# Kernel tuning notes

Measured on AMD Instinct MI355X. Metric: run time of the kernel, lower is better.

The kernel has to match this reference:

```python
import jax, jax.numpy as jnp
import numpy as np

ATT_HEAD, IN_DIM, OUT_DIM = 8, 768, 96
B, N = 8, 1024
LEAKY_ALPHA = 0.2


def setup_inputs() -> dict:
    key = jax.random.key(0)
    ks = jax.random.split(key, 8)
    feat_in = jax.random.normal(ks[0], (B, N, IN_DIM), dtype=jnp.float32)
    adj = jax.random.randint(ks[1], (B, N, N), 0, 2).astype(jnp.float32)
    # xavier-ish init scales
    W = jax.random.normal(ks[2], (ATT_HEAD, IN_DIM, OUT_DIM), dtype=jnp.float32) * (1.0 / np.sqrt(IN_DIM))
    b = jnp.zeros((OUT_DIM,), dtype=jnp.float32)
    w_src = jax.random.normal(ks[3], (ATT_HEAD, OUT_DIM, 1), dtype=jnp.float32) * (1.0 / np.sqrt(OUT_DIM))
    w_dst = jax.random.normal(ks[4], (ATT_HEAD, OUT_DIM, 1), dtype=jnp.float32) * (1.0 / np.sqrt(OUT_DIM))
    Hw = jax.random.normal(ks[5], (IN_DIM, IN_DIM), dtype=jnp.float32) * (1.0 / np.sqrt(IN_DIM))
    Hb = jnp.zeros((IN_DIM,), dtype=jnp.float32)
    return {"feat_in": feat_in, "adj": adj, "W": W, "b": b,
            "w_src": w_src, "w_dst": w_dst, "Hw": Hw, "Hb": Hb}


def reference(feat_in, adj, W, b, w_src, w_dst, Hw, Hb):
    batch, n, _ = feat_in.shape
    # per-head projection: [B,H,N,O]
    h = jnp.einsum('bni,hio->bhno', feat_in, W)
    t = jnp.tanh(h)
    a_src = jnp.einsum('bhno,hoq->bhnq', t, w_src)[..., 0]  # [B,H,N]
    a_dst = jnp.einsum('bhno,hoq->bhnq', t, w_dst)[..., 0]  # [B,H,N]
    attn = a_src[:, :, :, None] + a_dst[:, :, None, :]       # [B,H,N,N]
    attn = jnp.where(attn >= 0, attn, LEAKY_ALPHA * attn)
    mask = adj[:, None, :, :] == 0                            # 1-adj as bool
    attn = jnp.where(mask, jnp.float32(-999.0), attn)
    attn = jax.nn.softmax(attn, axis=-1)
    feat_out = jnp.einsum('bhnm,bhmo->bhno', attn, h) + b     # [B,H,N,O]
    feat_out = jnp.transpose(feat_out, (0, 2, 1, 3)).reshape(batch, n, -1)
    feat_out = jax.nn.elu(feat_out)
    gate = jax.nn.sigmoid(feat_in @ Hw.T + Hb)
    return gate * feat_out + (1.0 - gate) * feat_in
```

## Files before the change

kernel.cpp:

```cpp
#include <hip/hip_runtime.h>
#include <cstddef>

#define BATCH 8
#define NN 1024
#define IN_DIM 768
#define OUT_DIM 96
#define HEADS 8
#define M_ROWS 8192
#define NCOLS 1536

typedef __attribute__((ext_vector_type(8))) short short8;
typedef __attribute__((ext_vector_type(4))) float f32x4;
typedef __attribute__((ext_vector_type(4))) unsigned short ushort4v;
typedef _Float16 half8 __attribute__((ext_vector_type(8)));

typedef __attribute__((address_space(1))) void gvoid_t;
typedef __attribute__((address_space(3))) void lvoid_t;

__device__ __forceinline__ void gload_lds16(const void* g, void* l) {
    __builtin_amdgcn_global_load_lds((gvoid_t*)(unsigned long long)g,
                                     (lvoid_t*)(unsigned int)(unsigned long long)l,
                                     16, 0, 0);
}

__device__ __forceinline__ unsigned int pkrtz(float a, float b) {
    return __builtin_bit_cast(unsigned int, __builtin_amdgcn_cvt_pkrtz(a, b));
}
__device__ __forceinline__ unsigned short f2h(float x) {
    _Float16 h = (_Float16)x;
    return __builtin_bit_cast(unsigned short, h);
}
__device__ __forceinline__ float h2f(unsigned short u) {
    return (float)__builtin_bit_cast(_Float16, u);
}
__device__ __forceinline__ float tanh_fast(float x) {
    return 1.f - 2.f / (__expf(2.f * x) + 1.f);
}
__device__ __forceinline__ f32x4 mfma16(short8 a, short8 b, f32x4 c) {
    return __builtin_amdgcn_mfma_f32_16x16x32_f16(
        __builtin_bit_cast(half8, a), __builtin_bit_cast(half8, b), c, 0, 0, 0);
}

__global__ __launch_bounds__(256) void prep_kernel(
        const float* __restrict__ feat_in, const float* __restrict__ W,
        const float* __restrict__ Hw, const float* __restrict__ adj,
        unsigned short* __restrict__ Xb, unsigned short* __restrict__ BT,
        unsigned int* __restrict__ abits, float* __restrict__ a_zero) {
    int blk = blockIdx.x;
    int t = threadIdx.x;
    if (blk < 3072) {
        int idx = blk * 256 + t;
        const float4* p = (const float4*)(feat_in + (size_t)idx * 8);
        float4 a = p[0], b = p[1];
        union { unsigned int u4[4]; short8 s8; } pk;
        pk.u4[0] = pkrtz(a.x, a.y);
        pk.u4[1] = pkrtz(a.z, a.w);
        pk.u4[2] = pkrtz(b.x, b.y);
        pk.u4[3] = pkrtz(b.z, b.w);
        *(short8*)(Xb + (size_t)idx * 8) = pk.s8;
    } else if (blk < 5376) {
        int idx = (blk - 3072) * 256 + t;
        int c = idx / IN_DIM, i = idx % IN_DIM;
        int h = c / OUT_DIM, o = c % OUT_DIM;
        BT[(size_t)c * IN_DIM + i] = f2h(W[((size_t)h * IN_DIM + i) * OUT_DIM + o]);
    } else if (blk < 7680) {
        int idx = (blk - 5376) * 256 + t;
        int c = idx / IN_DIM, i = idx % IN_DIM;
        BT[(size_t)(768 + c) * IN_DIM + i] = f2h(Hw[(size_t)c * IN_DIM + i]);
    } else if (blk < 8704) {
        int idx = (blk - 7680) * 256 + t;
        const float4* p = (const float4*)(adj + (size_t)idx * 32);
        unsigned int m = 0;
        #pragma unroll
        for (int q = 0; q < 8; ++q) {
            float4 v = p[q];
            m |= (v.x != 0.f ? 1u : 0u) << (q * 4 + 0);
            m |= (v.y != 0.f ? 1u : 0u) << (q * 4 + 1);
            m |= (v.z != 0.f ? 1u : 0u) << (q * 4 + 2);
            m |= (v.w != 0.f ? 1u : 0u) << (q * 4 + 3);
        }
        abits[idx] = m;
    } else {
        int idx = (blk - 8704) * 256 + t;
        f32x4 z = {0.f, 0.f, 0.f, 0.f};
        *(f32x4*)(a_zero + (size_t)idx * 8) = z;
        *(f32x4*)(a_zero + (size_t)idx * 8 + 4) = z;
    }
}

__global__ __launch_bounds__(256) void gemm1_kernel(
        const unsigned short* __restrict__ Xb, const unsigned short* __restrict__ BT,
        const float* __restrict__ Hb, const float* __restrict__ w_src,
        const float* __restrict__ w_dst,
        unsigned short* __restrict__ h_bt, unsigned short* __restrict__ gate,
        float* __restrict__ a_src, float* __restrict__ a_dst) {
    __shared__ __align__(16) unsigned short As[128 * 64];
    __shared__ __align__(16) unsigned short Bs[128 * 64];
    __shared__ float hbs[128];
    __shared__ float ws_s[128], wd_s[128];
    int m0 = blockIdx.x * 128;
    int c0 = blockIdx.y * 128;
    int t = threadIdx.x;
    int w = t >> 6, lane = t & 63, l15 = t & 15, quad = lane >> 4;
    if (c0 >= 768) {
        if (t < 128) hbs[t] = Hb[c0 - 768 + t];
    } else {
        if (t < 128) {
            int c = c0 + t;
            int hd = c / OUT_DIM, o = c % OUT_DIM;
            ws_s[t] = w_src[hd * OUT_DIM + o];
            wd_s[t] = w_dst[hd * OUT_DIM + o];
        }
    }
    f32x4 acc[2][8] = {};
    for (int k0 = 0; k0 < IN_DIM; k0 += 64) {
        __syncthreads();
        #pragma unroll
        for (int cc = 0; cc < 4; ++cc) {
            int base64 = (w * 4 + cc) * 64;
            int p = base64 + lane;
            int r = p >> 3, qs = p & 7;
            int qb = qs ^ (r & 7);
            gload_lds16(Xb + (size_t)(m0 + r) * IN_DIM + k0 + qb * 8, As + base64 * 8);
            gload_lds16(BT + (size_t)(c0 + r) * IN_DIM + k0 + qb * 8, Bs + base64 * 8);
        }
        __syncthreads();
        #pragma unroll
        for (int ks = 0; ks < 2; ++ks) {
            short8 af[2], bfr[8];
            #pragma unroll
            for (int mt = 0; mt < 2; ++mt) {
                int r = w * 32 + mt * 16 + l15;
                int cb = (ks * 4 + quad) ^ (r & 7);
                af[mt] = *(const short8*)(As + r * 64 + cb * 8);
            }
            #pragma unroll
            for (int nt = 0; nt < 8; ++nt) {
                int r = nt * 16 + l15;
                int cb = (ks * 4 + quad) ^ (r & 7);
                bfr[nt] = *(const short8*)(Bs + r * 64 + cb * 8);
            }
            #pragma unroll
            for (int mt = 0; mt < 2; ++mt)
                #pragma unroll
                for (int nt = 0; nt < 8; ++nt)
                    acc[mt][nt] = mfma16(af[mt], bfr[nt], acc[mt][nt]);
        }
    }
    int b = m0 >> 10;
    if (c0 < 768) {
        int split = (c0 / 96 + 1) * 96 - c0;
        int headlo = c0 / 96;
        #pragma unroll
        for (int mt = 0; mt < 2; ++mt) {
            int rowbase = m0 + w * 32 + mt * 16 + quad * 4;
            int nbase = rowbase & 1023;
            #pragma unroll
            for (int nt = 0; nt < 8; ++nt) {
                int c = c0 + nt * 16 + l15;
                int hh = c / OUT_DIM, o = c % OUT_DIM;
                union { unsigned int u2[2]; ushort4v u4; } pk;
                pk.u2[0] = pkrtz(acc[mt][nt][0], acc[mt][nt][1]);
                pk.u2[1] = pkrtz(acc[mt][nt][2], acc[mt][nt][3]);
                *(ushort4v*)(h_bt + ((size_t)(b * 8 + hh) * OUT_DIM + o) * NN + nbase) = pk.u4;
            }
            #pragma unroll
            for (int reg = 0; reg < 4; ++reg) {
                float psA = 0.f, pdA = 0.f, psB = 0.f, pdB = 0.f;
                #pragma unroll
                for (int nt = 0; nt < 8; ++nt) {
                    int cl = nt * 16 + l15;
                    float th = tanh_fast(acc[mt][nt][reg]);
                    float s = th * ws_s[cl], d = th * wd_s[cl];
                    if (cl < split) { psA += s; pdA += d; }
                    else            { psB += s; pdB += d; }
                }
                #pragma unroll
                for (int mk = 1; mk <= 8; mk <<= 1) {
                    psA += __shfl_xor(psA, mk); pdA += __shfl_xor(pdA, mk);
                    psB += __shfl_xor(psB, mk); pdB += __shfl_xor(pdB, mk);
                }
                if (l15 == 0) {
                    int n2 = nbase + reg;
                    int ilo = (b * 8 + headlo) * 1024 + n2;
                    atomicAdd(&a_src[ilo], psA * 1.44269504f);
                    atomicAdd(&a_dst[ilo], pdA * 1.44269504f);
                    atomicAdd(&a_src[ilo + 1024], psB * 1.44269504f);
                    atomicAdd(&a_dst[ilo + 1024], pdB * 1.44269504f);
                }
            }
        }
    } else {
        #pragma unroll
        for (int mt = 0; mt < 2; ++mt) {
            int rowbase = m0 + w * 32 + mt * 16 + quad * 4;
            #pragma unroll
            for (int nt = 0; nt < 8; ++nt) {
                int cl = nt * 16 + l15;
                int cg = c0 - 768 + cl;
                #pragma unroll
                for (int reg = 0; reg < 4; ++reg) {
                    float z = acc[mt][nt][reg] + hbs[cl];
                    float g = __builtin_amdgcn_rcpf(1.f + __builtin_amdgcn_exp2f(-1.44269504f * z));
                    gate[(size_t)(rowbase + reg) * 768 + cg] = f2h(g);
                }
            }
        }
    }
}

__global__ __launch_bounds__(512) void attn_kernel(
        const unsigned short* __restrict__ h_bt, const unsigned int* __restrict__ abits,
        const float* __restrict__ a_src_g, const float* __restrict__ a_dst_g,
        const unsigned short* __restrict__ gate, const unsigned short* __restrict__ Xb,
        const float* __restrict__ bias, float* __restrict__ out) {
    __shared__ __align__(16) unsigned short hs[2][96 * 64];
    __shared__ __align__(16) float adst[1024];
    __shared__ float bias_s[96];
    int blk = blockIdx.x;
    int bh = (blk & 7) * 8 + ((blk >> 3) & 7);
    int i0 = (blk >> 6) * 128;
    int b = bh >> 3, hh = bh & 7;
    int t = threadIdx.x;
    int w = t >> 6, lane = t & 63, l15 = t & 15, quad = lane >> 4;
    if (t < 256) *(f32x4*)(adst + t * 4) = *(const f32x4*)(a_dst_g + bh * 1024 + t * 4);
    if (t < 96) bias_s[t] = bias[t];
    int irow = i0 + w * 16 + l15;
    float si = a_src_g[bh * 1024 + irow];
    const unsigned short* hhp = h_bt + (size_t)bh * 96 * NN;
    if (w < 6) {
        #pragma unroll
        for (int cc = 0; cc < 2; ++cc) {
            int u0 = (w * 2 + cc) * 64;
            int p = u0 + lane;
            int r = p >> 3, qs = p & 7, qb = qs ^ (r & 7);
            gload_lds16(hhp + (size_t)r * NN + qb * 8, (char*)&hs[0][0] + (size_t)u0 * 16);
        }
    }
    const unsigned int* mrow = abits + ((size_t)b * NN + irow) * 32;
    uint2 mw = *(const uint2*)(mrow);
    f32x4 acc[7] = {};
    short8 ones = {};
    if (l15 == 0) {
        #pragma unroll
        for (int u = 0; u < 8; ++u) ones[u] = (short)0x3C00;
    }
    __syncthreads();
    for (int j0 = 0; j0 < 1024; j0 += 64) {
        int cur = (j0 >> 6) & 1;
        int jn = j0 + 64;
        if (jn < 1024 && w < 6) {
            #pragma unroll
            for (int cc = 0; cc < 2; ++cc) {
                int u0 = (w * 2 + cc) * 64;
                int p = u0 + lane;
                int r = p >> 3, qs = p & 7, qb = qs ^ (r & 7);
                gload_lds16(hhp + (size_t)r * NN + jn + qb * 8, (char*)&hs[cur ^ 1][0] + (size_t)u0 * 16);
            }
        }
        short8 af[2];
        unsigned int mws[2] = {mw.x, mw.y};
        #pragma unroll
        for (int ks = 0; ks < 2; ++ks) {
            unsigned int byte = (mws[ks] >> (quad * 8)) & 0xFFu;
            f32x4 d0 = *(const f32x4*)(&adst[j0 + ks * 32 + quad * 8]);
            f32x4 d1 = *(const f32x4*)(&adst[j0 + ks * 32 + quad * 8 + 4]);
            float dv[8] = {d0[0], d0[1], d0[2], d0[3], d1[0], d1[1], d1[2], d1[3]};
            float ev[8];
            #pragma unroll
            for (int u = 0; u < 8; ++u) {
                float s = si + dv[u];
                float l = fmaxf(s, 0.2f * s);
                float e = __builtin_amdgcn_exp2f(l);
                ev[u] = ((byte >> u) & 1u) ? e : 0.f;
            }
            union { unsigned int u4[4]; short8 s8; } pk;
            pk.u4[0] = pkrtz(ev[0], ev[1]);
            pk.u4[1] = pkrtz(ev[2], ev[3]);
            pk.u4[2] = pkrtz(ev[4], ev[5]);
            pk.u4[3] = pkrtz(ev[6], ev[7]);
            af[ks] = pk.s8;
        }
        if (jn < 1024) mw = *(const uint2*)(mrow + (jn >> 5));
        #pragma unroll
        for (int ks = 0; ks < 2; ++ks) {
            #pragma unroll
            for (int nt = 0; nt < 6; ++nt) {
                int r = nt * 16 + l15;
                int qs = (ks * 4 + quad) ^ (r & 7);
                short8 bfr = *(const short8*)(&hs[cur][(size_t)(r * 8 + qs) * 8]);
                acc[nt] = mfma16(af[ks], bfr, acc[nt]);
            }
            acc[6] = mfma16(af[ks], ones, acc[6]);
        }
        __syncthreads();
    }
    int rowq = i0 + w * 16 + quad * 4;
    #pragma unroll
    for (int reg = 0; reg < 4; ++reg) {
        float ssum = __shfl(acc[6][reg], (lane & 48));
        float inv = (ssum > 0.f) ? __builtin_amdgcn_rcpf(ssum) : 0.f;
        int n = rowq + reg;
        size_t mrow_o = ((size_t)b * NN + n) * 768 + hh * 96;
        #pragma unroll
        for (int nt = 0; nt < 6; ++nt) {
            int cl = nt * 16 + l15;
            float v = acc[nt][reg] * inv + bias_s[cl];
            float e = (v > 0.f) ? v : (__builtin_amdgcn_exp2f(v * 1.44269504f) - 1.f);
            float g = h2f(gate[mrow_o + cl]);
            float x = h2f(Xb[mrow_o + cl]);
            out[mrow_o + cl] = x + g * (e - x);
        }
    }
}

extern "C" void kernel_launch(void* const* d_in, const int* in_sizes, int n_in,
                              void* d_out, int out_size, void* d_ws, size_t ws_size,
                              hipStream_t stream) {
    const float* feat_in = (const float*)d_in[0];
    const float* adj     = (const float*)d_in[1];
    const float* W       = (const float*)d_in[2];
    const float* bbias   = (const float*)d_in[3];
    const float* w_src   = (const float*)d_in[4];
    const float* w_dst   = (const float*)d_in[5];
    const float* Hw      = (const float*)d_in[6];
    const float* Hb      = (const float*)d_in[7];
    float* out = (float*)d_out;
    char* base = (char*)d_ws;

    unsigned short* Xb    = (unsigned short*)(base);
    unsigned short* BcatT = (unsigned short*)(base + 12582912);
    unsigned short* h_bt  = (unsigned short*)(base + 14942208);
    unsigned short* gate  = (unsigned short*)(base + 27525120);
    float* a_src = (float*)(base + 40108032);
    float* a_dst = (float*)(base + 40370176);
    unsigned int* abits = (unsigned int*)(base + 40632320);

    prep_kernel<<<8768, 256, 0, stream>>>(feat_in, W, Hw, adj, Xb, BcatT, abits, a_src);
    gemm1_kernel<<<dim3(M_ROWS / 128, NCOLS / 128), 256, 0, stream>>>(
        Xb, BcatT, Hb, w_src, w_dst, h_bt, gate, a_src, a_dst);
    attn_kernel<<<64 * 8, 512, 0, stream>>>(h_bt, abits, a_src, a_dst, gate, Xb, bbias, out);
}
```

Measured before the change: 185.3 us.

## Double-buffer gemm1 LDS tiles with 32-wide K steps to overlap loads

Replaces the single-buffered 64-wide K loop in gemm1 with two 32-wide LDS buffers. The global-to-LDS load for the next K slice is issued before the MFMA work on the current slice, so memory latency is meant to hide behind compute. The XOR swizzle is dropped in favour of an unswizzled 32-column layout, which may bring LDS bank conflicts back. The step count doubles and the number of barriers per unit of work goes up.

```diff
diff --git a/kernel.cpp b/kernel.cpp
--- a/kernel.cpp
+++ b/kernel.cpp
@@ -94,8 +94,8 @@
         const float* __restrict__ w_dst,
         unsigned short* __restrict__ h_bt, unsigned short* __restrict__ gate,
         float* __restrict__ a_src, float* __restrict__ a_dst) {
-    __shared__ __align__(16) unsigned short As[128 * 64];
-    __shared__ __align__(16) unsigned short Bs[128 * 64];
+    __shared__ __align__(16) unsigned short As[2][128 * 32];
+    __shared__ __align__(16) unsigned short Bs[2][128 * 32];
     __shared__ float hbs[128];
     __shared__ float ws_s[128], wd_s[128];
     int m0 = blockIdx.x * 128;
@@ -112,41 +112,47 @@
             wd_s[t] = w_dst[hd * OUT_DIM + o];
         }
     }
+    int uA0 = w * 2, uA1 = w * 2 + 1;
+    int rA0 = uA0 * 16 + (lane >> 2), rA1 = uA1 * 16 + (lane >> 2);
+    int qo = (lane & 3) * 8;
+    const unsigned short* gA0 = Xb + (size_t)(m0 + rA0) * IN_DIM + qo;
+    const unsigned short* gA1 = Xb + (size_t)(m0 + rA1) * IN_DIM + qo;
+    const unsigned short* gB0 = BT + (size_t)(c0 + rA0) * IN_DIM + qo;
+    const unsigned short* gB1 = BT + (size_t)(c0 + rA1) * IN_DIM + qo;
+    int aoff0 = (w * 32 + l15) * 32 + quad * 8;
+    int aoff1 = aoff0 + 16 * 32;
+    int boff  = l15 * 32 + quad * 8;
+
     f32x4 acc[2][8] = {};
-    for (int k0 = 0; k0 < IN_DIM; k0 += 64) {
+
+    auto stage = [&](unsigned short* Ad, unsigned short* Bd, int koff) {
+        gload_lds16(gA0 + koff, Ad + uA0 * 512);
+        gload_lds16(gA1 + koff, Ad + uA1 * 512);
+        gload_lds16(gB0 + koff, Bd + uA0 * 512);
+        gload_lds16(gB1 + koff, Bd + uA1 * 512);
+    };
+    auto compute = [&](const unsigned short* Ab, const unsigned short* Bb) {
+        short8 af0 = *(const short8*)(Ab + aoff0);
+        short8 af1 = *(const short8*)(Ab + aoff1);
+        #pragma unroll
+        for (int nt = 0; nt < 8; ++nt) {
+            short8 bfr = *(const short8*)(Bb + boff + nt * 512);
+            acc[0][nt] = mfma16(af0, bfr, acc[0][nt]);
+            acc[1][nt] = mfma16(af1, bfr, acc[1][nt]);
+        }
+    };
+
+    stage(&As[0][0], &Bs[0][0], 0);
+    __syncthreads();
+    for (int ts = 0; ts < 24; ts += 2) {
+        stage(&As[1][0], &Bs[1][0], (ts + 1) * 32);
+        compute(&As[0][0], &Bs[0][0]);
         __syncthreads();
-        #pragma unroll
-        for (int cc = 0; cc < 4; ++cc) {
-            int base64 = (w * 4 + cc) * 64;
-            int p = base64 + lane;
-            int r = p >> 3, qs = p & 7;
-            int qb = qs ^ (r & 7);
-            gload_lds16(Xb + (size_t)(m0 + r) * IN_DIM + k0 + qb * 8, As + base64 * 8);
-            gload_lds16(BT + (size_t)(c0 + r) * IN_DIM + k0 + qb * 8, Bs + base64 * 8);
-        }
+        if (ts + 2 < 24) stage(&As[0][0], &Bs[0][0], (ts + 2) * 32);
+        compute(&As[1][0], &Bs[1][0]);
         __syncthreads();
-        #pragma unroll
-        for (int ks = 0; ks < 2; ++ks) {
-            short8 af[2], bfr[8];
-            #pragma unroll
-            for (int mt = 0; mt < 2; ++mt) {
-                int r = w * 32 + mt * 16 + l15;
-                int cb = (ks * 4 + quad) ^ (r & 7);
-                af[mt] = *(const short8*)(As + r * 64 + cb * 8);
-            }
-            #pragma unroll
-            for (int nt = 0; nt < 8; ++nt) {
-                int r = nt * 16 + l15;
-                int cb = (ks * 4 + quad) ^ (r & 7);
-                bfr[nt] = *(const short8*)(Bs + r * 64 + cb * 8);
-            }
-            #pragma unroll
-            for (int mt = 0; mt < 2; ++mt)
-                #pragma unroll
-                for (int nt = 0; nt < 8; ++nt)
-                    acc[mt][nt] = mfma16(af[mt], bfr[nt], acc[mt][nt]);
-        }
-    }
+    }
+
     int b = m0 >> 10;
     if (c0 < 768) {
         int split = (c0 / 96 + 1) * 96 - c0;
```

Result: no change. 188.1 us (+1.5%).
